# Optimization experiments

Measured on AMD Instinct MI355X. Metric: run time of the kernel, lower is better.

## Reference

```python
import jax, jax.numpy as jnp
import numpy as np

B = 1
T, H, W = 8, 20, 20
N = T * H * W  # 3200
DIM = 3072
NH = 24
HD = DIM // NH  # 128
D_T, D_H, D_W = 32, 48, 48  # 3D RoPE split of head_dim
EPS = 1e-6


def _axis_freqs(d, n):
    # [n, d//2] angles for one axis
    inv = 1.0 / (10000.0 ** (jnp.arange(0, d, 2, dtype=jnp.float32) / d))
    return jnp.arange(n, dtype=jnp.float32)[:, None] * inv[None, :]


def rope3d_cos_sin(t, h, w):
    ft = jnp.broadcast_to(_axis_freqs(D_T, t)[:, None, None, :], (t, h, w, D_T // 2))
    fh = jnp.broadcast_to(_axis_freqs(D_H, h)[None, :, None, :], (t, h, w, D_H // 2))
    fw = jnp.broadcast_to(_axis_freqs(D_W, w)[None, None, :, :], (t, h, w, D_W // 2))
    f = jnp.concatenate([ft, fh, fw], axis=-1).reshape(t * h * w, HD // 2)
    return jnp.cos(f), jnp.sin(f)


def apply_rope(x, cos, sin):
    # x: [B, N, NH, HD]; interleaved pairs rotation
    xf = x.astype(jnp.float32).reshape(*x.shape[:-1], HD // 2, 2)
    x1, x2 = xf[..., 0], xf[..., 1]
    c = cos[None, :, None, :]
    s = sin[None, :, None, :]
    r1 = x1 * c - x2 * s
    r2 = x1 * s + x2 * c
    return jnp.stack([r1, r2], axis=-1).reshape(x.shape).astype(x.dtype)


def rmsnorm(x, w):
    xf = x.astype(jnp.float32)
    n = xf * jax.lax.rsqrt(jnp.mean(xf * xf, axis=-1, keepdims=True) + EPS)
    return (n * w).astype(x.dtype)


def setup_inputs() -> dict:
    key = jax.random.key(0)
    ks = jax.random.split(key, 6)
    scale = 0.02
    return {
        "x": jax.random.normal(ks[0], (B, N, DIM), jnp.float32),
        "Wq": jax.random.normal(ks[1], (DIM, DIM), jnp.float32) * scale,
        "bq": jnp.zeros((DIM,), jnp.float32),
        "Wk": jax.random.normal(ks[2], (DIM, DIM), jnp.float32) * scale,
        "bk": jnp.zeros((DIM,), jnp.float32),
        "Wv": jax.random.normal(ks[3], (DIM, DIM), jnp.float32) * scale,
        "bv": jnp.zeros((DIM,), jnp.float32),
        "Wo": jax.random.normal(ks[4], (DIM, DIM), jnp.float32) * scale,
        "bo": jnp.zeros((DIM,), jnp.float32),
        "q_norm_w": jnp.ones((HD,), jnp.float32),
        "k_norm_w": jnp.ones((HD,), jnp.float32),
        "num_cond_latents": 2,
    }


def reference(x, Wq, bq, Wk, bk, Wv, bv, Wo, bo, q_norm_w, k_norm_w, num_cond_latents):
    # QKV projections -> [B, N, NH, HD]
    q = (x @ Wq + bq).reshape(B, N, NH, HD)
    k = (x @ Wk + bk).reshape(B, N, NH, HD)
    v = (x @ Wv + bv).reshape(B, N, NH, HD)
    # per-head RMSNorm on q, k
    q = rmsnorm(q, q_norm_w)
    k = rmsnorm(k, k_norm_w)
    # 3D RoPE over (T, H, W) grid
    cos, sin = rope3d_cos_sin(T, H, W)
    q = apply_rope(q, cos, sin)
    k = apply_rope(k, cos, sin)
    # I2V split: cond tokens attend only to themselves; noise tokens attend to all
    nct = num_cond_latents * (N // T)  # static python int
    out_cond = jax.nn.dot_product_attention(q[:, :nct], k[:, :nct], v[:, :nct])
    out_noise = jax.nn.dot_product_attention(q[:, nct:], k, v)
    out = jnp.concatenate([out_cond, out_noise], axis=1).reshape(B, N, DIM)
    return out @ Wo + bo
```

## Files before the change

kernel.cpp:

```cpp
#include <hip/hip_runtime.h>
#include <stdint.h>

typedef _Float16 f16;
typedef _Float16 f16x2 __attribute__((ext_vector_type(2)));
typedef _Float16 f16x4 __attribute__((ext_vector_type(4)));
typedef _Float16 f16x8 __attribute__((ext_vector_type(8)));
typedef float f32x4 __attribute__((ext_vector_type(4)));
typedef float f32x16 __attribute__((ext_vector_type(16)));

#define DIM   3072
#define NTOK  3200
#define NHEAD 24
#define SCALE 0.08838834764831845f
#define LOG2E 1.4426950408889634f

__device__ __forceinline__ void async16(const void* g, void* l) {
  __builtin_amdgcn_global_load_lds(
      (const __attribute__((address_space(1))) uint32_t*)g,
      (__attribute__((address_space(3))) uint32_t*)l, 16, 0, 0);
}

__device__ __forceinline__ uint32_t pkrtz(float a, float b) {
  auto p = __builtin_amdgcn_cvt_pkrtz(a, b);
  return __builtin_bit_cast(uint32_t, p);
}

__device__ __forceinline__ float fexp2(float x) {
  float r;
  asm("v_exp_f32 %0, %1" : "=v"(r) : "v"(x));
  return r;
}

__device__ __forceinline__ f32x4 mfma16(f16x8 a, f16x8 b, f32x4 c) {
  return __builtin_amdgcn_mfma_f32_16x16x32_f16(a, b, c, 0, 0, 0);
}


__global__ __launch_bounds__(256) void cvt_f32_f16(const float* __restrict__ in,
                                                   f16* __restrict__ out) {
  size_t i = ((size_t)blockIdx.x * 256 + threadIdx.x) * 4;
  float4 v = *(const float4*)(in + i);
  f16x4 o = {(f16)v.x, (f16)v.y, (f16)v.z, (f16)v.w};
  *(f16x4*)(out + i) = o;
}

__global__ __launch_bounds__(256) void transpose4(
    const float* __restrict__ W0, const float* __restrict__ W1,
    const float* __restrict__ W2, const float* __restrict__ W3,
    f16* __restrict__ T0, f16* __restrict__ T1,
    f16* __restrict__ T2, f16* __restrict__ T3) {
  const float* W; f16* T;
  switch (blockIdx.z) {
    case 0: W = W0; T = T0; break;
    case 1: W = W1; T = T1; break;
    case 2: W = W2; T = T2; break;
    default: W = W3; T = T3; break;
  }
  __shared__ float t[32][33];
  int tx = threadIdx.x & 31, ty = threadIdx.x >> 5;
  size_t bx = (size_t)blockIdx.x * 32, by = (size_t)blockIdx.y * 32;
#pragma unroll
  for (int r = 0; r < 4; ++r)
    t[ty + r * 8][tx] = W[(by + ty + r * 8) * DIM + bx + tx];
  __syncthreads();
#pragma unroll
  for (int r = 0; r < 4; ++r)
    T[(bx + ty + r * 8) * DIM + by + tx] = (f16)t[tx][ty + r * 8];
}

__global__ __launch_bounds__(256) void rope_tables(float* __restrict__ cosT,
                                                   float* __restrict__ sinT) {
  int tid = blockIdx.x * 256 + threadIdx.x;
  int p = tid >> 6, j = tid & 63;
  int t = p / 400, rem = p % 400;
  int hh = rem / 20, ww = rem % 20;
  float val, e;
  if (j < 16)      { val = (float)t;  e = (float)(2 * j)        * (1.f / 32.f); }
  else if (j < 40) { val = (float)hh; e = (float)(2 * (j - 16)) * (1.f / 48.f); }
  else             { val = (float)ww; e = (float)(2 * (j - 40)) * (1.f / 48.f); }
  float f = val * expf(-e * 9.210340371976184f);
  cosT[tid] = cosf(f);
  sinT[tid] = sinf(f);
}


__device__ __forceinline__ void stage_half(const f16* __restrict__ base, int row0,
                                           int rowmax, int k0, char* ldsdst, int tid) {
#pragma unroll
  for (int s = 0; s < 2; ++s) {
    int idx = s * 512 + tid;
    int r = idx >> 3, pc = idx & 7;
    int cc = pc ^ (r & 7);
    int grow = row0 + r;
    grow = grow < rowmax ? grow : rowmax - 1;
    async16(base + (size_t)grow * DIM + k0 + cc * 8, ldsdst + idx * 16);
  }
}

__device__ __forceinline__ void gemm256_body(
    const f16* __restrict__ A, const f16* __restrict__ Bm,
    const float* __restrict__ bias, void* __restrict__ C,
    int m0, int n0, int Mrows, int mode, char* smem) {

  const int tid = threadIdx.x;
  const int lane = tid & 63, w = tid >> 6;
  const int wm = w >> 2, wn = w & 3;
  const int l15 = lane & 15, l4 = lane >> 4;

  f32x4 acc[8][4];
#pragma unroll
  for (int m = 0; m < 8; ++m)
#pragma unroll
    for (int n = 0; n < 4; ++n) acc[m][n] = (f32x4){0.f, 0.f, 0.f, 0.f};

  const int NT = DIM / 64;

  stage_half(A,  m0,       Mrows,   0,  smem + 0,     tid);
  stage_half(Bm, n0,       1 << 30, 0,  smem + 32768, tid);
  stage_half(A,  m0 + 128, Mrows,   0,  smem + 16384, tid);
  stage_half(Bm, n0 + 128, 1 << 30, 0,  smem + 49152, tid);
  stage_half(A,  m0,       Mrows,   64, smem + 65536, tid);
  asm volatile("s_waitcnt vmcnt(2)" ::: "memory");
  __builtin_amdgcn_s_barrier();

  const int arow0 = wm * 128 + l15;
  const int brow0 = wn * 64 + l15;

  for (int t = 0; t < NT; ++t) {
    char* bufc = smem + (t & 1) * 65536;
    char* bufn = smem + ((t + 1) & 1) * 65536;
    const f16* Ald = (const f16*)bufc;
    const f16* Bld = (const f16*)(bufc + 32768);
    int k1 = (t + 1) * 64; k1 = k1 <= DIM - 64 ? k1 : DIM - 64;
    int k2 = (t + 2) * 64; k2 = k2 <= DIM - 64 ? k2 : DIM - 64;

    f16x8 af[8], b0, b1;

#pragma unroll
    for (int m = 0; m < 8; ++m) {
      int r = arow0 + m * 16, pc = l4 ^ (r & 7);
      af[m] = *(const f16x8*)(Ald + r * 64 + pc * 8);
    }
    { int r = brow0,      pc = l4 ^ (r & 7); b0 = *(const f16x8*)(Bld + r * 64 + pc * 8);
      r = brow0 + 16;     pc = l4 ^ (r & 7); b1 = *(const f16x8*)(Bld + r * 64 + pc * 8); }
    stage_half(Bm, n0, 1 << 30, k1, bufn + 32768, tid);
    __builtin_amdgcn_s_barrier();
    asm volatile("s_waitcnt lgkmcnt(0)" ::: "memory");
    __builtin_amdgcn_sched_barrier(0);
    __builtin_amdgcn_s_setprio(1);
#pragma unroll
    for (int m = 0; m < 8; ++m) {
      acc[m][0] = mfma16(af[m], b0, acc[m][0]);
      acc[m][1] = mfma16(af[m], b1, acc[m][1]);
    }
    __builtin_amdgcn_s_setprio(0);
    __builtin_amdgcn_s_barrier();

    { int r = brow0 + 32, pc = l4 ^ (r & 7); b0 = *(const f16x8*)(Bld + r * 64 + pc * 8);
      r = brow0 + 48;     pc = l4 ^ (r & 7); b1 = *(const f16x8*)(Bld + r * 64 + pc * 8); }
    stage_half(A, m0 + 128, Mrows, k1, bufn + 16384, tid);
    __builtin_amdgcn_s_barrier();
    asm volatile("s_waitcnt lgkmcnt(0)" ::: "memory");
    __builtin_amdgcn_sched_barrier(0);
    __builtin_amdgcn_s_setprio(1);
#pragma unroll
    for (int m = 0; m < 8; ++m) {
      acc[m][2] = mfma16(af[m], b0, acc[m][2]);
      acc[m][3] = mfma16(af[m], b1, acc[m][3]);
    }
    __builtin_amdgcn_s_setprio(0);
    __builtin_amdgcn_s_barrier();

#pragma unroll
    for (int m = 0; m < 8; ++m) {
      int r = arow0 + m * 16, pc = (4 + l4) ^ (r & 7);
      af[m] = *(const f16x8*)(Ald + r * 64 + pc * 8);
    }
    { int r = brow0,      pc = (4 + l4) ^ (r & 7); b0 = *(const f16x8*)(Bld + r * 64 + pc * 8);
      r = brow0 + 16;     pc = (4 + l4) ^ (r & 7); b1 = *(const f16x8*)(Bld + r * 64 + pc * 8); }
    stage_half(Bm, n0 + 128, 1 << 30, k1, bufn + 49152, tid);
    __builtin_amdgcn_s_barrier();
    asm volatile("s_waitcnt lgkmcnt(0)" ::: "memory");
    __builtin_amdgcn_sched_barrier(0);
    __builtin_amdgcn_s_setprio(1);
#pragma unroll
    for (int m = 0; m < 8; ++m) {
      acc[m][0] = mfma16(af[m], b0, acc[m][0]);
      acc[m][1] = mfma16(af[m], b1, acc[m][1]);
    }
    __builtin_amdgcn_s_setprio(0);
    __builtin_amdgcn_s_barrier();

    { int r = brow0 + 32, pc = (4 + l4) ^ (r & 7); b0 = *(const f16x8*)(Bld + r * 64 + pc * 8);
      r = brow0 + 48;     pc = (4 + l4) ^ (r & 7); b1 = *(const f16x8*)(Bld + r * 64 + pc * 8); }
    stage_half(A, m0, Mrows, k2, bufc + 0, tid);
    __builtin_amdgcn_s_barrier();
    asm volatile("s_waitcnt lgkmcnt(0)" ::: "memory");
    __builtin_amdgcn_sched_barrier(0);
    __builtin_amdgcn_s_setprio(1);
#pragma unroll
    for (int m = 0; m < 8; ++m) {
      acc[m][2] = mfma16(af[m], b0, acc[m][2]);
      acc[m][3] = mfma16(af[m], b1, acc[m][3]);
    }
    __builtin_amdgcn_s_setprio(0);
    asm volatile("s_waitcnt vmcnt(2)" ::: "memory");
    __builtin_amdgcn_s_barrier();
  }

#pragma unroll
  for (int n = 0; n < 4; ++n) {
    int col = n0 + wn * 64 + n * 16 + l15;
    float bb = bias[col];
#pragma unroll
    for (int m = 0; m < 8; ++m) {
      int rbase = m0 + wm * 128 + m * 16 + l4 * 4;
      if (rbase < Mrows) {
        if (mode == 2) {
          f16x4 ov;
#pragma unroll
          for (int r = 0; r < 4; ++r) ov[r] = (f16)(acc[m][n][r] + bb);
          *(f16x4*)((f16*)C + (size_t)col * NTOK + rbase) = ov;
        } else if (mode == 1) {
#pragma unroll
          for (int r = 0; r < 4; ++r)
            ((float*)C)[(size_t)(rbase + r) * DIM + col] = acc[m][n][r] + bb;
        } else {
#pragma unroll
          for (int r = 0; r < 4; ++r)
            ((f16*)C)[(size_t)(rbase + r) * DIM + col] = (f16)(acc[m][n][r] + bb);
        }
      }
    }
  }
}

__global__ __launch_bounds__(512, 2) void gemm256_qkv(
    const f16* __restrict__ A,
    const f16* __restrict__ B0, const f16* __restrict__ B1, const f16* __restrict__ B2,
    const float* __restrict__ b0, const float* __restrict__ b1, const float* __restrict__ b2,
    f16* __restrict__ C0, f16* __restrict__ C1, f16* __restrict__ C2) {
  __shared__ char smem[131072];
  int sel = blockIdx.y / 12, yn = blockIdx.y % 12;
  const f16* B = sel == 0 ? B0 : (sel == 1 ? B1 : B2);
  const float* bias = sel == 0 ? b0 : (sel == 1 ? b1 : b2);
  f16* C = sel == 0 ? C0 : (sel == 1 ? C1 : C2);
  gemm256_body(A, B, bias, C, blockIdx.x * 256, yn * 256, NTOK, sel == 2 ? 2 : 0, smem);
}

__global__ __launch_bounds__(512, 2) void gemm256_out(
    const f16* __restrict__ A, const f16* __restrict__ B,
    const float* __restrict__ bias, float* __restrict__ C) {
  __shared__ char smem[131072];
  gemm256_body(A, B, bias, C, blockIdx.x * 256, blockIdx.y * 256, NTOK, 1, smem);
}

__global__ __launch_bounds__(256) void rmsnorm_rope2(
    f16* __restrict__ qbuf, f16* __restrict__ kbuf,
    const float* __restrict__ qw, const float* __restrict__ kw,
    const float* __restrict__ cosT, const float* __restrict__ sinT) {
  f16* qk = blockIdx.y ? kbuf : qbuf;
  const float* w = blockIdx.y ? kw : qw;
  const float osc = blockIdx.y ? 1.0f : SCALE * LOG2E;
  int lane = threadIdx.x & 63, rb = threadIdx.x >> 6;
  int row = blockIdx.x * 4 + rb;
  int p = row / NHEAD;
  f16* ptr = qk + (size_t)row * 128 + lane * 2;
  f16x2 hv = *(const f16x2*)ptr;
  float x1 = (float)hv[0], x2 = (float)hv[1];
  float ss = x1 * x1 + x2 * x2;
#pragma unroll
  for (int o = 32; o > 0; o >>= 1) ss += __shfl_xor(ss, o);
  float r = rsqrtf(ss * (1.f / 128.f) + 1e-6f);
  float n1 = x1 * r * w[lane * 2], n2 = x2 * r * w[lane * 2 + 1];
  float c = cosT[p * 64 + lane], s = sinT[p * 64 + lane];
  f16x2 ov = {(f16)((n1 * c - n2 * s) * osc), (f16)((n1 * s + n2 * c) * osc)};
  *(f16x2*)ptr = ov;
}

__global__ __launch_bounds__(320) void attn5(
    const f16* __restrict__ q, const f16* __restrict__ k, const f16* __restrict__ vt,
    f16* __restrict__ out) {
  __shared__ char smem[65536];
  f16* Ks = (f16*)smem;
  f16* Vs = (f16*)(smem + 32768);

  int L = blockIdx.x;
  int c = L & 7, j = L >> 3;
  int head = c * 3 + j / 20, qblk = j % 20;
  int q0 = qblk * 160;
  int kv_len = (q0 < 800) ? 800 : 3200;

  const int tid = threadIdx.x, lane = tid & 63, w = tid >> 6;
  const int l31 = lane & 31, hi = lane >> 5;
  const int qg = q0 + w * 32 + l31;
  const int sw_base = l31 & 15;

  f16x8 qr[8];
#pragma unroll
  for (int ks = 0; ks < 8; ++ks)
    qr[ks] = *(const f16x8*)(q + (size_t)qg * DIM + head * 128 + ks * 16 + hi * 8);

  const f16x8 ones = {(f16)1, (f16)1, (f16)1, (f16)1, (f16)1, (f16)1, (f16)1, (f16)1};

  f32x16 o[4], lsum;
#pragma unroll
  for (int mb = 0; mb < 4; ++mb)
#pragma unroll
    for (int r = 0; r < 16; ++r) o[mb][r] = 0.f;
#pragma unroll
  for (int r = 0; r < 16; ++r) lsum[r] = 0.f;
  float m_run = -1e30f;

  for (int t0 = 0; t0 < kv_len; t0 += 128) {
    __syncthreads();
#pragma unroll
    for (int r = 0; r < 13; ++r) {
      int idx = r * 320 + tid;
      if (idx < 4096) {
        int row = (idx >> 4) & 127;
        int sw = (idx & 15) ^ (row & 15);
        const f16* src;
        if (idx < 2048) src = k + (size_t)(t0 + row) * DIM + head * 128 + sw * 8;
        else            src = vt + ((size_t)head * 128 + row) * NTOK + t0 + sw * 8;
        async16(src, smem + idx * 16);
      }
    }
    __syncthreads();

    const int nvb = min(4, (kv_len - t0) >> 5);

    f32x16 s4[4];
#pragma unroll
    for (int b = 0; b < 4; ++b)
#pragma unroll
      for (int r = 0; r < 16; ++r) s4[b][r] = 0.f;
    __builtin_amdgcn_s_setprio(1);
#pragma unroll
    for (int ks = 0; ks < 8; ++ks) {
#pragma unroll
      for (int b = 0; b < 4; ++b) {
        if (b < nvb) {
          const f16x8 kf = *(const f16x8*)(Ks + ((b * 32 + l31) << 7) +
                                           (((ks * 2 + hi) ^ sw_base) << 3));
          s4[b] = __builtin_amdgcn_mfma_f32_32x32x16_f16(kf, qr[ks], s4[b], 0, 0, 0);
        }
      }
    }
    __builtin_amdgcn_s_setprio(0);

    float tmax = -1e30f;
#pragma unroll
    for (int b = 0; b < 4; ++b)
      if (b < nvb)
#pragma unroll
        for (int r = 0; r < 16; r += 2)
          tmax = fmaxf(tmax, fmaxf(s4[b][r], s4[b][r + 1]));
    tmax = fmaxf(tmax, __shfl_xor(tmax, 32));
    if (!__all(tmax <= m_run + 11.54f)) {
      float mn = fmaxf(m_run, tmax);
      float alpha = fexp2(m_run - mn);
#pragma unroll
      for (int mb = 0; mb < 4; ++mb)
#pragma unroll
        for (int r = 0; r < 16; ++r) o[mb][r] *= alpha;
#pragma unroll
      for (int r = 0; r < 16; ++r) lsum[r] *= alpha;
      m_run = mn;
    }
#pragma unroll
    for (int b = 0; b < 4; ++b)
      if (b < nvb)
#pragma unroll
        for (int r = 0; r < 16; ++r)
          s4[b][r] = fexp2(s4[b][r] - m_run);

    const int nks = nvb * 2;
#pragma unroll
    for (int ks = 0; ks < 8; ++ks) {
      if (ks < nks) {
        const int b = ks >> 1, s8 = (ks & 1) * 8;
        uint32_t a0 = pkrtz(s4[b][s8 + 0], s4[b][s8 + 1]);
        uint32_t b0 = pkrtz(s4[b][s8 + 4], s4[b][s8 + 5]);
        asm("v_permlane32_swap_b32 %0, %1" : "+v"(a0), "+v"(b0));
        uint32_t a1 = pkrtz(s4[b][s8 + 2], s4[b][s8 + 3]);
        uint32_t b1 = pkrtz(s4[b][s8 + 6], s4[b][s8 + 7]);
        asm("v_permlane32_swap_b32 %0, %1" : "+v"(a1), "+v"(b1));
        union { uint32_t u[4]; f16x8 v; } pf;
        pf.u[0] = a0; pf.u[1] = a1; pf.u[2] = b0; pf.u[3] = b1;
        __builtin_amdgcn_s_setprio(1);
#pragma unroll
        for (int mb = 0; mb < 4; ++mb) {
          const f16x8 vf = *(const f16x8*)(Vs + ((mb * 32 + l31) << 7) +
                                           (((ks * 2 + hi) ^ sw_base) << 3));
          o[mb] = __builtin_amdgcn_mfma_f32_32x32x16_f16(vf, pf.v, o[mb], 0, 0, 0);
        }
        lsum = __builtin_amdgcn_mfma_f32_32x32x16_f16(ones, pf.v, lsum, 0, 0, 0);
        __builtin_amdgcn_s_setprio(0);
      }
    }
  }

  float inv = 1.f / lsum[0];
#pragma unroll
  for (int mb = 0; mb < 4; ++mb)
#pragma unroll
    for (int jq = 0; jq < 4; ++jq) {
      f16x4 ov;
#pragma unroll
      for (int e = 0; e < 4; ++e) ov[e] = (f16)(o[mb][jq * 4 + e] * inv);
      *(f16x4*)(out + (size_t)qg * DIM + head * 128 + mb * 32 + jq * 8 + hi * 4) = ov;
    }
}


extern "C" void kernel_launch(void* const* d_in, const int* in_sizes, int n_in,
                              void* d_out, int out_size, void* d_ws, size_t ws_size,
                              hipStream_t stream) {
  const float* x   = (const float*)d_in[0];
  const float* Wq  = (const float*)d_in[1];
  const float* bq  = (const float*)d_in[2];
  const float* Wk  = (const float*)d_in[3];
  const float* bk  = (const float*)d_in[4];
  const float* Wv  = (const float*)d_in[5];
  const float* bv  = (const float*)d_in[6];
  const float* Wo  = (const float*)d_in[7];
  const float* bo  = (const float*)d_in[8];
  const float* qnw = (const float*)d_in[9];
  const float* knw = (const float*)d_in[10];

  char* ws = (char*)d_ws;
  f16*   xb   = (f16*)(ws);
  f16*   WqT  = (f16*)(ws + 19660800);
  f16*   WkT  = (f16*)(ws + 38535168);
  f16*   WvT  = (f16*)(ws + 57409536);
  f16*   WoT  = (f16*)(ws + 76283904);
  f16*   qb   = (f16*)(ws + 95158272);
  f16*   kb   = (f16*)(ws + 114819072);
  f16*   vtb  = (f16*)(ws + 134479872);
  f16*   ab   = (f16*)(ws + 154140672);
  float* cosT = (float*)(ws + 173801472);
  float* sinT = (float*)(ws + 174620672);

  cvt_f32_f16<<<9600, 256, 0, stream>>>(x, xb);
  transpose4<<<dim3(96, 96, 4), 256, 0, stream>>>(Wq, Wk, Wv, Wo, WqT, WkT, WvT, WoT);
  rope_tables<<<800, 256, 0, stream>>>(cosT, sinT);

  gemm256_qkv<<<dim3(13, 36), 512, 0, stream>>>(xb, WqT, WkT, WvT, bq, bk, bv, qb, kb, vtb);

  rmsnorm_rope2<<<dim3(19200, 2), 256, 0, stream>>>(qb, kb, qnw, knw, cosT, sinT);

  attn5<<<480, 320, 0, stream>>>(qb, kb, vtb, ab);

  gemm256_out<<<dim3(13, 12), 512, 0, stream>>>(ab, WoT, bo, (float*)d_out);
}
```

Measured before the change: 568.8 us.

## Split KV range for noise-token attention and merge partials in a separate kernel

Noise-token query blocks, which attend over all 3200 keys, are split into two halves of the key range. This raises the grid from 480 to 840 more evenly sized blocks, reducing wave-quantization tail imbalance across CUs. Each split writes a normalized partial output plus its running max and sum. A new merge kernel combines the two partials with log-sum-exp weights. The cost is an extra kernel launch and extra global traffic for the partial outputs, which reuse dead workspace regions.

```diff
diff --git a/kernel.cpp b/kernel.cpp
--- a/kernel.cpp
+++ b/kernel.cpp
@@ -278,18 +278,25 @@
   *(f16x2*)ptr = ov;
 }
 
-__global__ __launch_bounds__(320) void attn5(
+__global__ __launch_bounds__(320) void attn6(
     const f16* __restrict__ q, const f16* __restrict__ k, const f16* __restrict__ vt,
-    f16* __restrict__ out) {
+    f16* __restrict__ out, f16* __restrict__ Op, float2* __restrict__ ml) {
   __shared__ char smem[65536];
   f16* Ks = (f16*)smem;
   f16* Vs = (f16*)(smem + 32768);
 
   int L = blockIdx.x;
-  int c = L & 7, j = L >> 3;
-  int head = c * 3 + j / 20, qblk = j % 20;
-  int q0 = qblk * 160;
-  int kv_len = (q0 < 800) ? 800 : 3200;
+  int xcd = L & 7, j = L >> 3;
+  int head = xcd * 3 + j / 35;
+  int u = j % 35;
+  int q0, kv_lo, kv_hi, s = 0;
+  bool direct;
+  if (u < 5) { q0 = u * 160; kv_lo = 0; kv_hi = 800; direct = true; }
+  else {
+    int v = u - 5;
+    int qn = v >> 1; s = v & 1;
+    q0 = 800 + qn * 160; kv_lo = s * 1600; kv_hi = kv_lo + 1600; direct = false;
+  }
 
   const int tid = threadIdx.x, lane = tid & 63, w = tid >> 6;
   const int l31 = lane & 31, hi = lane >> 5;
@@ -312,7 +319,7 @@
   for (int r = 0; r < 16; ++r) lsum[r] = 0.f;
   float m_run = -1e30f;
 
-  for (int t0 = 0; t0 < kv_len; t0 += 128) {
+  for (int t0 = kv_lo; t0 < kv_hi; t0 += 128) {
     __syncthreads();
 #pragma unroll
     for (int r = 0; r < 13; ++r) {
@@ -328,7 +335,7 @@
     }
     __syncthreads();
 
-    const int nvb = min(4, (kv_len - t0) >> 5);
+    const int nvb = min(4, (kv_hi - t0) >> 5);
 
     f32x16 s4[4];
 #pragma unroll
@@ -402,6 +409,9 @@
   }
 
   float inv = 1.f / lsum[0];
+  f16* obase = direct
+      ? out + (size_t)qg * DIM + head * 128
+      : Op + ((size_t)(s * NHEAD + head) * 2400 + (qg - 800)) * 128;
 #pragma unroll
   for (int mb = 0; mb < 4; ++mb)
 #pragma unroll
@@ -409,8 +419,30 @@
       f16x4 ov;
 #pragma unroll
       for (int e = 0; e < 4; ++e) ov[e] = (f16)(o[mb][jq * 4 + e] * inv);
-      *(f16x4*)(out + (size_t)qg * DIM + head * 128 + mb * 32 + jq * 8 + hi * 4) = ov;
-    }
+      *(f16x4*)(obase + mb * 32 + jq * 8 + hi * 4) = ov;
+    }
+  if (!direct && hi == 0)
+    ml[(size_t)(s * NHEAD + head) * 2400 + (qg - 800)] = make_float2(m_run, lsum[0]);
+}
+
+__global__ __launch_bounds__(256) void attn_merge(
+    const f16* __restrict__ Op, const float2* __restrict__ ml,
+    f16* __restrict__ out) {
+  int row = blockIdx.x * 4 + (threadIdx.x >> 6);
+  int lane = threadIdx.x & 63;
+  int head = row / 2400, qn = row % 2400;
+  float2 ml1 = ml[row];
+  float2 ml2 = ml[24 * 2400 + row];
+  float m = fmaxf(ml1.x, ml2.x);
+  float w1 = ml1.y * fexp2(ml1.x - m);
+  float w2 = ml2.y * fexp2(ml2.x - m);
+  float inv = 1.f / (w1 + w2);
+  w1 *= inv; w2 *= inv;
+  f16x2 o1 = *(const f16x2*)(Op + (size_t)row * 128 + lane * 2);
+  f16x2 o2 = *(const f16x2*)(Op + (size_t)(24 * 2400 + row) * 128 + lane * 2);
+  f16x2 ov = {(f16)((float)o1[0] * w1 + (float)o2[0] * w2),
+              (f16)((float)o1[1] * w1 + (float)o2[1] * w2)};
+  *(f16x2*)(out + (size_t)(800 + qn) * DIM + head * 128 + lane * 2) = ov;
 }
 
 
@@ -441,6 +473,8 @@
   f16*   ab   = (f16*)(ws + 154140672);
   float* cosT = (float*)(ws + 173801472);
   float* sinT = (float*)(ws + 174620672);
+  f16*    Op  = (f16*)(ws);
+  float2* ml  = (float2*)(ws + 29491200);
 
   cvt_f32_f16<<<9600, 256, 0, stream>>>(x, xb);
   transpose4<<<dim3(96, 96, 4), 256, 0, stream>>>(Wq, Wk, Wv, Wo, WqT, WkT, WvT, WoT);
@@ -450,7 +484,8 @@
 
   rmsnorm_rope2<<<dim3(19200, 2), 256, 0, stream>>>(qb, kb, qnw, knw, cosT, sinT);
 
-  attn5<<<480, 320, 0, stream>>>(qb, kb, vtb, ab);
+  attn6<<<840, 320, 0, stream>>>(qb, kb, vtb, ab, Op, ml);
+  attn_merge<<<14400, 256, 0, stream>>>(Op, ml, ab);
 
   gemm256_out<<<dim3(13, 12), 512, 0, stream>>>(ab, WoT, bo, (float*)d_out);
 }
```

After: 559.2 us. Within noise of the previous version (-1.7%).
